# Performance work log

Measured on AMD Instinct MI355X. Metric: run time of the kernel, lower is better.

## Reference

```python
import jax, jax.numpy as jnp
import numpy as np

B, H, T, D, R = 2, 12, 2048, 64, 16
D_STD = D - R


def setup_inputs() -> dict:
    key = jax.random.key(0)
    ks = jax.random.split(key, 5)
    return {
        "Q": jax.random.normal(ks[0], (B, H, T, D), jnp.float32),
        "K": jax.random.normal(ks[1], (B, H, T, D), jnp.float32),
        "V": jax.random.normal(ks[2], (B, H, T, D), jnp.float32),
        "d_bias": jax.random.normal(ks[3], (B, H, T), jnp.float32),
        "W_recip": jax.random.normal(ks[4], (D, R), jnp.float32) * 0.02,
        "w_std": jnp.full((H,), 0.5, jnp.float32),
        "w_rec": jnp.full((H,), 0.3, jnp.float32),
        "w_disc": jnp.full((H,), 0.2, jnp.float32),
    }


def reference(Q, K, V, d_bias, W_recip, w_std, w_rec, w_disc):
    b, h, t, d = Q.shape
    r = W_recip.shape[1]
    d_std = d - r
    sq_std = jnp.sqrt(w_std)[None, :, None, None]  # [1,H,1,1]
    sq_rec = jnp.sqrt(w_rec)[None, :, None, None]
    Q_low = jnp.einsum("bhtd,dr->bhtr", Q, W_recip)  # [B,H,T,R]
    K_low = jnp.einsum("bhtd,dr->bhtr", K, W_recip)
    Q_aug = jnp.concatenate([sq_std * Q[..., :d_std], sq_rec * K_low], axis=-1)  # [B,H,T,D]
    K_aug = jnp.concatenate([sq_std * K[..., :d_std], sq_rec * Q_low], axis=-1)
    scale = 1.0 / jnp.sqrt(jnp.asarray(d, Q.dtype))
    scores = jnp.einsum("bhqd,bhkd->bhqk", Q_aug, K_aug) * scale  # [B,H,T,T]
    # rank-1 additive bias, broadcast over queries: bias[b,h,q,k] = w_disc[h]*d_bias[b,h,k]
    scores = scores + (w_disc[None, :, None, None] * d_bias[:, :, None, :])
    causal = jnp.tril(jnp.ones((t, t), bool))  # [T,T]
    scores = jnp.where(causal[None, None], scores, -jnp.inf)
    attn = jax.nn.softmax(scores, axis=-1)
    return jnp.einsum("bhqk,bhkd->bhqd", attn, V)
```

## Files before the change

kernel.cpp:

```cpp
#include <hip/hip_runtime.h>
#include <math.h>

#define T_SEQ 2048
#define NH    12
#define NB    2
#define BHC   (NB*NH)
#define NQT   32

typedef _Float16 half4_t __attribute__((ext_vector_type(4)));
typedef _Float16 half8_t __attribute__((ext_vector_type(8)));
typedef float    floatx4 __attribute__((ext_vector_type(4)));

__device__ __forceinline__ half8_t h8splat(_Float16 s) {
  return (half8_t){s, s, s, s, s, s, s, s};
}

__global__ __launch_bounds__(256) void prep_kernel(
    const float* __restrict__ Q, const float* __restrict__ K,
    const float* __restrict__ V, const float* __restrict__ W,
    const float* __restrict__ wstd, const float* __restrict__ wrec,
    const float* __restrict__ dbias, const float* __restrict__ wdisc,
    ushort* __restrict__ QF, ushort* __restrict__ KF, ushort* __restrict__ VF,
    float* __restrict__ B2)
{
  __shared__ __align__(16) _Float16 Qsh[64*72];
  __shared__ __align__(16) _Float16 Ksh[64*72];
  __shared__ __align__(16) _Float16 Vsh[64*72];
  __shared__ __align__(16) _Float16 Lqh[64*16];
  __shared__ __align__(16) _Float16 Lkh[64*16];

  const int tid = threadIdx.x;
  const int w = tid >> 6, lane = tid & 63;
  const int quad = lane >> 4, ln = lane & 15;
  const int bh = blockIdx.x >> 5, tblk = blockIdx.x & 31;
  const long g0 = ((long)bh * T_SEQ + tblk * 64) * 64;

  const float4* gQ = (const float4*)(Q + g0);
  const float4* gK = (const float4*)(K + g0);
  const float4* gV = (const float4*)(V + g0);
  for (int i = tid; i < 1024; i += 256) {
    int r = i >> 4, c4 = i & 15;
    float4 q = gQ[i], k = gK[i], v = gV[i];
    *(half4_t*)&Qsh[r*72 + c4*4] = (half4_t){(_Float16)q.x,(_Float16)q.y,(_Float16)q.z,(_Float16)q.w};
    *(half4_t*)&Ksh[r*72 + c4*4] = (half4_t){(_Float16)k.x,(_Float16)k.y,(_Float16)k.z,(_Float16)k.w};
    *(half4_t*)&Vsh[r*72 + c4*4] = (half4_t){(_Float16)v.x,(_Float16)v.y,(_Float16)v.z,(_Float16)v.w};
  }
  __syncthreads();

  half4_t bw[4];
#pragma unroll
  for (int dk = 0; dk < 4; dk++)
#pragma unroll
    for (int i = 0; i < 4; i++)
      bw[dk][i] = (_Float16)W[(dk*16 + quad*4 + i)*16 + ln];

  floatx4 cq = {0.f,0.f,0.f,0.f}, ck = {0.f,0.f,0.f,0.f};
#pragma unroll
  for (int dk = 0; dk < 4; dk++) {
    half4_t aq = *(const half4_t*)&Qsh[(w*16 + ln)*72 + dk*16 + quad*4];
    half4_t ak = *(const half4_t*)&Ksh[(w*16 + ln)*72 + dk*16 + quad*4];
    cq = __builtin_amdgcn_mfma_f32_16x16x16f16(aq, bw[dk], cq, 0, 0, 0);
    ck = __builtin_amdgcn_mfma_f32_16x16x16f16(ak, bw[dk], ck, 0, 0, 0);
  }
#pragma unroll
  for (int i = 0; i < 4; i++) {
    Lqh[(w*16 + quad*4 + i)*16 + ln] = (_Float16)cq[i];
    Lkh[(w*16 + quad*4 + i)*16 + ln] = (_Float16)ck[i];
  }
  __syncthreads();

  const int h = bh % NH;
  const float sstd = sqrtf(wstd[h]);
  const float srec = sqrtf(wrec[h]);
  const half8_t hq_std = h8splat((_Float16)(0.125f * sstd));
  const half8_t hk_std = h8splat((_Float16)sstd);
  const half8_t hq_rec = h8splat((_Float16)(0.125f * srec));
  const half8_t hk_rec = h8splat((_Float16)srec);

  if (tid < 64) B2[(long)bh*T_SEQ + tblk*64 + tid] =
      wdisc[h] * dbias[(long)bh*T_SEQ + tblk*64 + tid];

#pragma unroll
  for (int cc = 0; cc < 2; cc++) {
    int c = tid + cc * 256;
    {
      int lp = c & 63, dp = (c >> 6) & 1, rt = c >> 7;
      int row = rt*16 + (lp & 15);
      int d0 = dp*32 + (lp >> 4)*8;
      half8_t hq, hk;
      if (d0 < 48) {
        hq = *(const half8_t*)&Qsh[row*72 + d0] * hq_std;
        hk = *(const half8_t*)&Ksh[row*72 + d0] * hk_std;
      } else {
        hq = *(const half8_t*)&Lkh[row*16 + (d0-48)] * hq_rec;
        hk = *(const half8_t*)&Lqh[row*16 + (d0-48)] * hk_rec;
      }
      long tile16 = (long)bh*128 + tblk*4 + rt;
      ((int4*)QF)[tile16*128 + dp*64 + lp] = *(int4*)&hq;
      ((int4*)KF)[tile16*128 + dp*64 + lp] = *(int4*)&hk;
    }
    {
      int lv = c & 63, nt = (c >> 6) & 3, v2 = c >> 8;
      int d = nt*16 + (lv & 15), qv = lv >> 4;
      half8_t hv;
#pragma unroll
      for (int j = 0; j < 4; j++) {
        hv[j]   = Vsh[(v2*32 + qv*4 + j)*72 + d];
        hv[4+j] = Vsh[(v2*32 + 16 + qv*4 + j)*72 + d];
      }
      ((int4*)VF)[((long)bh*32 + tblk)*512 + (v2*4 + nt)*64 + lv] = *(int4*)&hv;
    }
  }
}

__global__ __launch_bounds__(64, 4) void flash_kernel(
    const ushort* __restrict__ QF, const ushort* __restrict__ KF,
    const ushort* __restrict__ VF, const float* __restrict__ B2,
    float* __restrict__ Out)
{
  const int lane = threadIdx.x;
  const int quad = lane >> 4, ln = lane & 15;
  const int bid = blockIdx.x;
  const int bh  = bid % BHC;
  const int t16 = 127 - bid / BHC;
  const int qrow = t16*16 + ln;
  const int ktmax = t16 >> 2;

  const ushort* gK = KF + (long)bh * 131072;
  const ushort* gV = VF + (long)bh * 131072;
  const float*  gB = B2 + (long)bh * T_SEQ;

  half8_t bq[2];
  {
    const ushort* gQ = QF + ((long)bh*128 + t16) * 1024;
    bq[0] = *(const half8_t*)(gQ + lane*8);
    bq[1] = *(const half8_t*)(gQ + 512 + lane*8);
  }

  float m_i = -1e30f, l_i = 0.f;
  floatx4 acc[4];
#pragma unroll
  for (int nt = 0; nt < 4; nt++) acc[nt] = (floatx4){0.f,0.f,0.f,0.f};

  for (int kt = 0; kt <= ktmax; kt++) {
    const ushort* Kt = gK + (long)kt * 4096;
    const ushort* Vt = gV + (long)kt * 4096;

    floatx4 st[4];
#pragma unroll
    for (int mt = 0; mt < 4; mt++) {
      half8_t a0 = *(const half8_t*)(Kt + (mt*2    )*512 + lane*8);
      half8_t a1 = *(const half8_t*)(Kt + (mt*2 + 1)*512 + lane*8);
      floatx4 c = (floatx4){0.f,0.f,0.f,0.f};
      c = __builtin_amdgcn_mfma_f32_16x16x32_f16(a0, bq[0], c, 0, 0, 0);
      c = __builtin_amdgcn_mfma_f32_16x16x32_f16(a1, bq[1], c, 0, 0, 0);
      st[mt] = c;
    }

    const bool diag = (kt == ktmax);
    float rowmax = -1e30f;
#pragma unroll
    for (int mt = 0; mt < 4; mt++) {
      float4 bb = *(const float4*)(gB + kt*64 + mt*16 + quad*4);
      float bv[4] = {bb.x, bb.y, bb.z, bb.w};
#pragma unroll
      for (int i = 0; i < 4; i++) {
        float v = st[mt][i] + bv[i];
        int key = kt*64 + mt*16 + quad*4 + i;
        if (diag && key > qrow) v = -1e30f;
        st[mt][i] = v;
        rowmax = fmaxf(rowmax, v);
      }
    }
    rowmax = fmaxf(rowmax, __shfl_xor(rowmax, 16));
    rowmax = fmaxf(rowmax, __shfl_xor(rowmax, 32));
    float mnew  = fmaxf(m_i, rowmax);
    float alpha = __expf(m_i - mnew);
    float psum = 0.f;
    half4_t pa[4];
#pragma unroll
    for (int mt = 0; mt < 4; mt++)
#pragma unroll
      for (int i = 0; i < 4; i++) {
        float p = __expf(st[mt][i] - mnew);
        psum += p;
        pa[mt][i] = (_Float16)p;
      }
    psum += __shfl_xor(psum, 16);
    psum += __shfl_xor(psum, 32);
    l_i = l_i * alpha + psum;
    m_i = mnew;

    float af[4];
#pragma unroll
    for (int i = 0; i < 4; i++) af[i] = __shfl(alpha, quad*4 + i);
#pragma unroll
    for (int nt = 0; nt < 4; nt++)
#pragma unroll
      for (int i = 0; i < 4; i++) acc[nt][i] *= af[i];

#pragma unroll
    for (int v2 = 0; v2 < 2; v2++)
#pragma unroll
      for (int nt = 0; nt < 4; nt++) {
        half8_t vv = *(const half8_t*)(Vt + (v2*4 + nt)*512 + lane*8);
        half4_t b0 = __builtin_shufflevector(vv, vv, 0,1,2,3);
        half4_t b1 = __builtin_shufflevector(vv, vv, 4,5,6,7);
        acc[nt] = __builtin_amdgcn_mfma_f32_16x16x16f16(pa[2*v2],   b0, acc[nt], 0, 0, 0);
        acc[nt] = __builtin_amdgcn_mfma_f32_16x16x16f16(pa[2*v2+1], b1, acc[nt], 0, 0, 0);
      }
  }

  float lr[4];
#pragma unroll
  for (int i = 0; i < 4; i++) lr[i] = 1.f / __shfl(l_i, quad*4 + i);
  const long obase = (long)bh*T_SEQ*64 + (long)(t16*16)*64;
#pragma unroll
  for (int i = 0; i < 4; i++)
#pragma unroll
    for (int nt = 0; nt < 4; nt++)
      Out[obase + (quad*4 + i)*64 + nt*16 + ln] = acc[nt][i] * lr[i];
}

extern "C" void kernel_launch(void* const* d_in, const int* in_sizes, int n_in,
                              void* d_out, int out_size, void* d_ws, size_t ws_size,
                              hipStream_t stream) {
  const float* Q     = (const float*)d_in[0];
  const float* K     = (const float*)d_in[1];
  const float* V     = (const float*)d_in[2];
  const float* dbias = (const float*)d_in[3];
  const float* W     = (const float*)d_in[4];
  const float* wstd  = (const float*)d_in[5];
  const float* wrec  = (const float*)d_in[6];
  const float* wdisc = (const float*)d_in[7];
  float* Out = (float*)d_out;

  const long NEL = (long)BHC * T_SEQ * 64;
  ushort* QF = (ushort*)d_ws;
  ushort* KF = QF + NEL;
  ushort* VF = KF + NEL;
  float*  B2 = (float*)(VF + NEL);

  prep_kernel<<<BHC * NQT, 256, 0, stream>>>(Q, K, V, W, wstd, wrec, dbias, wdisc,
                                             QF, KF, VF, B2);
  flash_kernel<<<BHC * 128, 64, 0, stream>>>(QF, KF, VF, B2, Out);
}
```

Measured before the change: 135.3 us.

## Process two 16-row query tiles per wavefront to reuse K/V loads

Each flash wavefront now handles 32 query rows (two 16-row tiles) instead of 16, sharing every K and V fragment load between two sets of MFMAs and softmax states. This halves global K/V traffic per query and gives more independent MFMA chains to hide latency. In exchange it halves the grid size, roughly doubles register use (the occupancy hint in launch bounds is dropped), and the upper tile in each pair does some extra masked work on the diagonal block.

```diff
diff --git a/kernel.cpp b/kernel.cpp
--- a/kernel.cpp
+++ b/kernel.cpp
@@ -113,7 +113,7 @@
   }
 }
 
-__global__ __launch_bounds__(64, 4) void flash_kernel(
+__global__ __launch_bounds__(64) void flash_kernel(
     const ushort* __restrict__ QF, const ushort* __restrict__ KF,
     const ushort* __restrict__ VF, const float* __restrict__ B2,
     float* __restrict__ Out)
@@ -122,82 +122,101 @@
   const int quad = lane >> 4, ln = lane & 15;
   const int bid = blockIdx.x;
   const int bh  = bid % BHC;
-  const int t16 = 127 - bid / BHC;
-  const int qrow = t16*16 + ln;
-  const int ktmax = t16 >> 2;
+  const int u   = 63 - bid / BHC;
+  const int qrow_a = 32*u + ln;
+  const int qrow_b = qrow_a + 16;
+  const int ktmax = u >> 1;
 
   const ushort* gK = KF + (long)bh * 131072;
   const ushort* gV = VF + (long)bh * 131072;
   const float*  gB = B2 + (long)bh * T_SEQ;
 
-  half8_t bq[2];
+  half8_t bqa[2], bqb[2];
   {
-    const ushort* gQ = QF + ((long)bh*128 + t16) * 1024;
-    bq[0] = *(const half8_t*)(gQ + lane*8);
-    bq[1] = *(const half8_t*)(gQ + 512 + lane*8);
-  }
-
-  float m_i = -1e30f, l_i = 0.f;
-  floatx4 acc[4];
-#pragma unroll
-  for (int nt = 0; nt < 4; nt++) acc[nt] = (floatx4){0.f,0.f,0.f,0.f};
+    const ushort* gQa = QF + ((long)bh*128 + 2*u) * 1024;
+    bqa[0] = *(const half8_t*)(gQa + lane*8);
+    bqa[1] = *(const half8_t*)(gQa + 512 + lane*8);
+    bqb[0] = *(const half8_t*)(gQa + 1024 + lane*8);
+    bqb[1] = *(const half8_t*)(gQa + 1536 + lane*8);
+  }
+
+  float m_a = -1e30f, l_a = 0.f, m_b = -1e30f, l_b = 0.f;
+  floatx4 acca[4], accb[4];
+#pragma unroll
+  for (int nt = 0; nt < 4; nt++) {
+    acca[nt] = (floatx4){0.f,0.f,0.f,0.f};
+    accb[nt] = (floatx4){0.f,0.f,0.f,0.f};
+  }
 
   for (int kt = 0; kt <= ktmax; kt++) {
     const ushort* Kt = gK + (long)kt * 4096;
     const ushort* Vt = gV + (long)kt * 4096;
 
-    floatx4 st[4];
+    floatx4 sta[4], stb[4];
 #pragma unroll
     for (int mt = 0; mt < 4; mt++) {
       half8_t a0 = *(const half8_t*)(Kt + (mt*2    )*512 + lane*8);
       half8_t a1 = *(const half8_t*)(Kt + (mt*2 + 1)*512 + lane*8);
-      floatx4 c = (floatx4){0.f,0.f,0.f,0.f};
-      c = __builtin_amdgcn_mfma_f32_16x16x32_f16(a0, bq[0], c, 0, 0, 0);
-      c = __builtin_amdgcn_mfma_f32_16x16x32_f16(a1, bq[1], c, 0, 0, 0);
-      st[mt] = c;
+      floatx4 ca = (floatx4){0.f,0.f,0.f,0.f};
+      floatx4 cb = (floatx4){0.f,0.f,0.f,0.f};
+      ca = __builtin_amdgcn_mfma_f32_16x16x32_f16(a0, bqa[0], ca, 0, 0, 0);
+      cb = __builtin_amdgcn_mfma_f32_16x16x32_f16(a0, bqb[0], cb, 0, 0, 0);
+      ca = __builtin_amdgcn_mfma_f32_16x16x32_f16(a1, bqa[1], ca, 0, 0, 0);
+      cb = __builtin_amdgcn_mfma_f32_16x16x32_f16(a1, bqb[1], cb, 0, 0, 0);
+      sta[mt] = ca; stb[mt] = cb;
     }
 
     const bool diag = (kt == ktmax);
-    float rowmax = -1e30f;
+    float rma = -1e30f, rmb = -1e30f;
 #pragma unroll
     for (int mt = 0; mt < 4; mt++) {
       float4 bb = *(const float4*)(gB + kt*64 + mt*16 + quad*4);
       float bv[4] = {bb.x, bb.y, bb.z, bb.w};
 #pragma unroll
       for (int i = 0; i < 4; i++) {
-        float v = st[mt][i] + bv[i];
         int key = kt*64 + mt*16 + quad*4 + i;
-        if (diag && key > qrow) v = -1e30f;
-        st[mt][i] = v;
-        rowmax = fmaxf(rowmax, v);
-      }
-    }
-    rowmax = fmaxf(rowmax, __shfl_xor(rowmax, 16));
-    rowmax = fmaxf(rowmax, __shfl_xor(rowmax, 32));
-    float mnew  = fmaxf(m_i, rowmax);
-    float alpha = __expf(m_i - mnew);
-    float psum = 0.f;
-    half4_t pa[4];
+        float va = sta[mt][i] + bv[i];
+        float vb = stb[mt][i] + bv[i];
+        if (diag && key > qrow_a) va = -1e30f;
+        if (diag && key > qrow_b) vb = -1e30f;
+        sta[mt][i] = va; stb[mt][i] = vb;
+        rma = fmaxf(rma, va); rmb = fmaxf(rmb, vb);
+      }
+    }
+    rma = fmaxf(rma, __shfl_xor(rma, 16)); rma = fmaxf(rma, __shfl_xor(rma, 32));
+    rmb = fmaxf(rmb, __shfl_xor(rmb, 16)); rmb = fmaxf(rmb, __shfl_xor(rmb, 32));
+    float mna = fmaxf(m_a, rma), mnb = fmaxf(m_b, rmb);
+    float ala = __expf(m_a - mna), alb = __expf(m_b - mnb);
+    float psa = 0.f, psb = 0.f;
+    half4_t paa[4], pab[4];
 #pragma unroll
     for (int mt = 0; mt < 4; mt++)
 #pragma unroll
       for (int i = 0; i < 4; i++) {
-        float p = __expf(st[mt][i] - mnew);
-        psum += p;
-        pa[mt][i] = (_Float16)p;
-      }
-    psum += __shfl_xor(psum, 16);
-    psum += __shfl_xor(psum, 32);
-    l_i = l_i * alpha + psum;
-    m_i = mnew;
-
-    float af[4];
-#pragma unroll
-    for (int i = 0; i < 4; i++) af[i] = __shfl(alpha, quad*4 + i);
+        float pa = __expf(sta[mt][i] - mna);
+        float pb = __expf(stb[mt][i] - mnb);
+        psa += pa; psb += pb;
+        paa[mt][i] = (_Float16)pa;
+        pab[mt][i] = (_Float16)pb;
+      }
+    psa += __shfl_xor(psa, 16); psa += __shfl_xor(psa, 32);
+    psb += __shfl_xor(psb, 16); psb += __shfl_xor(psb, 32);
+    l_a = l_a * ala + psa;  m_a = mna;
+    l_b = l_b * alb + psb;  m_b = mnb;
+
+    float afa[4], afb[4];
+#pragma unroll
+    for (int i = 0; i < 4; i++) {
+      afa[i] = __shfl(ala, quad*4 + i);
+      afb[i] = __shfl(alb, quad*4 + i);
+    }
 #pragma unroll
     for (int nt = 0; nt < 4; nt++)
 #pragma unroll
-      for (int i = 0; i < 4; i++) acc[nt][i] *= af[i];
+      for (int i = 0; i < 4; i++) {
+        acca[nt][i] *= afa[i];
+        accb[nt][i] *= afb[i];
+      }
 
 #pragma unroll
     for (int v2 = 0; v2 < 2; v2++)
@@ -206,20 +225,27 @@
         half8_t vv = *(const half8_t*)(Vt + (v2*4 + nt)*512 + lane*8);
         half4_t b0 = __builtin_shufflevector(vv, vv, 0,1,2,3);
         half4_t b1 = __builtin_shufflevector(vv, vv, 4,5,6,7);
-        acc[nt] = __builtin_amdgcn_mfma_f32_16x16x16f16(pa[2*v2],   b0, acc[nt], 0, 0, 0);
-        acc[nt] = __builtin_amdgcn_mfma_f32_16x16x16f16(pa[2*v2+1], b1, acc[nt], 0, 0, 0);
-      }
-  }
-
-  float lr[4];
-#pragma unroll
-  for (int i = 0; i < 4; i++) lr[i] = 1.f / __shfl(l_i, quad*4 + i);
-  const long obase = (long)bh*T_SEQ*64 + (long)(t16*16)*64;
+        acca[nt] = __builtin_amdgcn_mfma_f32_16x16x16f16(paa[2*v2],   b0, acca[nt], 0, 0, 0);
+        accb[nt] = __builtin_amdgcn_mfma_f32_16x16x16f16(pab[2*v2],   b0, accb[nt], 0, 0, 0);
+        acca[nt] = __builtin_amdgcn_mfma_f32_16x16x16f16(paa[2*v2+1], b1, acca[nt], 0, 0, 0);
+        accb[nt] = __builtin_amdgcn_mfma_f32_16x16x16f16(pab[2*v2+1], b1, accb[nt], 0, 0, 0);
+      }
+  }
+
+  float lra[4], lrb[4];
+#pragma unroll
+  for (int i = 0; i < 4; i++) {
+    lra[i] = 1.f / __shfl(l_a, quad*4 + i);
+    lrb[i] = 1.f / __shfl(l_b, quad*4 + i);
+  }
+  const long obase = (long)bh*T_SEQ*64 + (long)(32*u)*64;
 #pragma unroll
   for (int i = 0; i < 4; i++)
 #pragma unroll
-    for (int nt = 0; nt < 4; nt++)
-      Out[obase + (quad*4 + i)*64 + nt*16 + ln] = acc[nt][i] * lr[i];
+    for (int nt = 0; nt < 4; nt++) {
+      Out[obase + (quad*4 + i)*64        + nt*16 + ln] = acca[nt][i] * lra[i];
+      Out[obase + (16 + quad*4 + i)*64   + nt*16 + ln] = accb[nt][i] * lrb[i];
+    }
 }
 
 extern "C" void kernel_launch(void* const* d_in, const int* in_sizes, int n_in,
@@ -243,5 +269,5 @@
 
   prep_kernel<<<BHC * NQT, 256, 0, stream>>>(Q, K, V, W, wstd, wrec, dbias, wdisc,
                                              QF, KF, VF, B2);
-  flash_kernel<<<BHC * 128, 64, 0, stream>>>(QF, KF, VF, B2, Out);
-}
+  flash_kernel<<<BHC * 64, 64, 0, stream>>>(QF, KF, VF, B2, Out);
+}
```

After: 223.6 us. 1.65x slower.

## Split causal attention along the KV axis into chunks and merge partial results

Applied to the files above, without the earlier changes.

Flash attention is restructured as split-KV. Causal work is divided into chunks of 8 key tiles, with diagonal and off-diagonal blocks scheduled separately over 256-thread blocks. Partial outputs are stored in fp16 together with m/l statistics, and a new merge kernel combines them. Smaller changes come along: log2e is folded into the Q scale and bias so exp2f can be used, the bias is preloaded into the MFMA accumulator, and K/V fragments are loaded ahead of use. The aim is better load balance and occupancy, at the cost of an extra kernel launch, workspace traffic, and fp16 rounding of the partials.

```diff
diff --git a/kernel.cpp b/kernel.cpp
--- a/kernel.cpp
+++ b/kernel.cpp
@@ -6,6 +6,7 @@
 #define NB    2
 #define BHC   (NB*NH)
 #define NQT   32
+#define LOG2E 1.44269504088896340736f
 
 typedef _Float16 half4_t __attribute__((ext_vector_type(4)));
 typedef _Float16 half8_t __attribute__((ext_vector_type(8)));
@@ -72,13 +73,14 @@
   const int h = bh % NH;
   const float sstd = sqrtf(wstd[h]);
   const float srec = sqrtf(wrec[h]);
-  const half8_t hq_std = h8splat((_Float16)(0.125f * sstd));
+  const float qsc  = 0.125f * LOG2E;
+  const half8_t hq_std = h8splat((_Float16)(qsc * sstd));
   const half8_t hk_std = h8splat((_Float16)sstd);
-  const half8_t hq_rec = h8splat((_Float16)(0.125f * srec));
+  const half8_t hq_rec = h8splat((_Float16)(qsc * srec));
   const half8_t hk_rec = h8splat((_Float16)srec);
 
   if (tid < 64) B2[(long)bh*T_SEQ + tblk*64 + tid] =
-      wdisc[h] * dbias[(long)bh*T_SEQ + tblk*64 + tid];
+      LOG2E * wdisc[h] * dbias[(long)bh*T_SEQ + tblk*64 + tid];
 
 #pragma unroll
   for (int cc = 0; cc < 2; cc++) {
@@ -113,113 +115,209 @@
   }
 }
 
-__global__ __launch_bounds__(64, 4) void flash_kernel(
+__global__ __launch_bounds__(256, 6) void flash_kernel(
     const ushort* __restrict__ QF, const ushort* __restrict__ KF,
     const ushort* __restrict__ VF, const float* __restrict__ B2,
+    ushort* __restrict__ P, float* __restrict__ ML,
+    float* __restrict__ Out)
+{
+  const int tid = threadIdx.x;
+  const int w = tid >> 6, lane = tid & 63;
+  const int quad = lane >> 4, ln = lane & 15;
+  const int bid = blockIdx.x;
+  const int bh  = bid % BHC;
+  const int rest = bid / BHC;
+  int c, j; bool diag;
+  if (rest < 48) {
+    if (rest < 24)      { c = 0; j = 8 + rest; }
+    else if (rest < 40) { c = 1; j = rest - 16; }
+    else                { c = 2; j = rest - 32; }
+    diag = false;
+  } else {
+    int d = rest - 48;
+    c = d & 3; j = 7 - (d >> 2);
+    diag = true;
+  }
+  const int t16 = 32*c + 4*j + w;
+  const int g   = 8*c + j;
+  const int k0  = 8*c;
+  const int nUn = diag ? j : 8;
+  const int qrow = t16*16 + ln;
+
+  const ushort* gK = KF + (long)bh * 131072;
+  const ushort* gV = VF + (long)bh * 131072;
+  const float*  gB = B2 + (long)bh * T_SEQ;
+
+  half8_t bq[2];
+  {
+    const ushort* gQ = QF + ((long)bh*128 + t16) * 1024;
+    bq[0] = *(const half8_t*)(gQ + lane*8);
+    bq[1] = *(const half8_t*)(gQ + 512 + lane*8);
+  }
+
+  float m_i = -1e30f, l_i = 0.f;
+  floatx4 acc[4];
+#pragma unroll
+  for (int nt = 0; nt < 4; nt++) acc[nt] = (floatx4){0.f,0.f,0.f,0.f};
+
+  auto body = [&](int kt, bool domask) {
+    const ushort* Kt = gK + (long)kt * 4096;
+    const ushort* Vt = gV + (long)kt * 4096;
+    float4 bbc[4];
+#pragma unroll
+    for (int mt = 0; mt < 4; mt++)
+      bbc[mt] = *(const float4*)(gB + kt*64 + mt*16 + quad*4);
+    half8_t kf[8];
+#pragma unroll
+    for (int cc = 0; cc < 8; cc++)
+      kf[cc] = *(const half8_t*)(Kt + cc*512 + lane*8);
+
+    floatx4 st[4];
+#pragma unroll
+    for (int mt = 0; mt < 4; mt++) {
+      floatx4 cc = (floatx4){bbc[mt].x, bbc[mt].y, bbc[mt].z, bbc[mt].w};
+      cc = __builtin_amdgcn_mfma_f32_16x16x32_f16(kf[mt*2],     bq[0], cc, 0, 0, 0);
+      cc = __builtin_amdgcn_mfma_f32_16x16x32_f16(kf[mt*2 + 1], bq[1], cc, 0, 0, 0);
+      st[mt] = cc;
+    }
+    half8_t vf[8];
+#pragma unroll
+    for (int cc = 0; cc < 8; cc++)
+      vf[cc] = *(const half8_t*)(Vt + cc*512 + lane*8);
+
+    float rowmax = -1e30f;
+#pragma unroll
+    for (int mt = 0; mt < 4; mt++)
+#pragma unroll
+      for (int i = 0; i < 4; i++) {
+        float v = st[mt][i];
+        if (domask) { int key = kt*64 + mt*16 + quad*4 + i; if (key > qrow) v = -1e30f; }
+        st[mt][i] = v;
+        rowmax = fmaxf(rowmax, v);
+      }
+    rowmax = fmaxf(rowmax, __shfl_xor(rowmax, 16));
+    rowmax = fmaxf(rowmax, __shfl_xor(rowmax, 32));
+    float mnew  = fmaxf(m_i, rowmax);
+    float alpha = exp2f(m_i - mnew);
+    float psum = 0.f;
+    half4_t pa[4];
+#pragma unroll
+    for (int mt = 0; mt < 4; mt++)
+#pragma unroll
+      for (int i = 0; i < 4; i++) {
+        float p = exp2f(st[mt][i] - mnew);
+        psum += p;
+        pa[mt][i] = (_Float16)p;
+      }
+    psum += __shfl_xor(psum, 16);
+    psum += __shfl_xor(psum, 32);
+    l_i = l_i * alpha + psum;
+    m_i = mnew;
+
+    float af[4];
+#pragma unroll
+    for (int i = 0; i < 4; i++) af[i] = __shfl(alpha, quad*4 + i);
+#pragma unroll
+    for (int nt = 0; nt < 4; nt++)
+#pragma unroll
+      for (int i = 0; i < 4; i++) acc[nt][i] *= af[i];
+
+#pragma unroll
+    for (int v2 = 0; v2 < 2; v2++)
+#pragma unroll
+      for (int nt = 0; nt < 4; nt++) {
+        half8_t vv = vf[v2*4 + nt];
+        half4_t b0 = __builtin_shufflevector(vv, vv, 0,1,2,3);
+        half4_t b1 = __builtin_shufflevector(vv, vv, 4,5,6,7);
+        acc[nt] = __builtin_amdgcn_mfma_f32_16x16x16f16(pa[2*v2],   b0, acc[nt], 0, 0, 0);
+        acc[nt] = __builtin_amdgcn_mfma_f32_16x16x16f16(pa[2*v2+1], b1, acc[nt], 0, 0, 0);
+      }
+  };
+
+  for (int it = 0; it < nUn; it++) body(k0 + it, false);
+  if (diag) body(g, true);
+
+  float lr[4];
+#pragma unroll
+  for (int i = 0; i < 4; i++) lr[i] = 1.f / __shfl(l_i, quad*4 + i);
+
+  if (diag && c == 0) {
+    const long obase = (long)bh*T_SEQ*64 + (long)(t16*16)*64;
+#pragma unroll
+    for (int i = 0; i < 4; i++)
+#pragma unroll
+      for (int nt = 0; nt < 4; nt++)
+        Out[obase + (quad*4 + i)*64 + nt*16 + ln] = acc[nt][i] * lr[i];
+  } else {
+    const int a = t16 >> 5, b = t16 & 31;
+    const int slot = bh*320 + t16 + 16*a*(a-1) + a*b + c;
+    half8_t h0, h1;
+#pragma unroll
+    for (int i = 0; i < 4; i++) {
+      h0[i]   = (_Float16)(acc[0][i] * lr[i]);
+      h0[4+i] = (_Float16)(acc[1][i] * lr[i]);
+      h1[i]   = (_Float16)(acc[2][i] * lr[i]);
+      h1[4+i] = (_Float16)(acc[3][i] * lr[i]);
+    }
+    *(int4*)&P[(long)slot*1024 + lane*16]     = *(int4*)&h0;
+    *(int4*)&P[(long)slot*1024 + lane*16 + 8] = *(int4*)&h1;
+    if (quad == 0) {
+      ML[slot*32 + ln]      = m_i;
+      ML[slot*32 + 16 + ln] = l_i;
+    }
+  }
+}
+
+__global__ __launch_bounds__(64) void merge_kernel(
+    const ushort* __restrict__ P, const float* __restrict__ ML,
     float* __restrict__ Out)
 {
   const int lane = threadIdx.x;
   const int quad = lane >> 4, ln = lane & 15;
   const int bid = blockIdx.x;
-  const int bh  = bid % BHC;
-  const int t16 = 127 - bid / BHC;
-  const int qrow = t16*16 + ln;
-  const int ktmax = t16 >> 2;
-
-  const ushort* gK = KF + (long)bh * 131072;
-  const ushort* gV = VF + (long)bh * 131072;
-  const float*  gB = B2 + (long)bh * T_SEQ;
-
-  half8_t bq[2];
-  {
-    const ushort* gQ = QF + ((long)bh*128 + t16) * 1024;
-    bq[0] = *(const half8_t*)(gQ + lane*8);
-    bq[1] = *(const half8_t*)(gQ + 512 + lane*8);
-  }
-
-  float m_i = -1e30f, l_i = 0.f;
-  floatx4 acc[4];
-#pragma unroll
-  for (int nt = 0; nt < 4; nt++) acc[nt] = (floatx4){0.f,0.f,0.f,0.f};
-
-  for (int kt = 0; kt <= ktmax; kt++) {
-    const ushort* Kt = gK + (long)kt * 4096;
-    const ushort* Vt = gV + (long)kt * 4096;
-
-    floatx4 st[4];
-#pragma unroll
-    for (int mt = 0; mt < 4; mt++) {
-      half8_t a0 = *(const half8_t*)(Kt + (mt*2    )*512 + lane*8);
-      half8_t a1 = *(const half8_t*)(Kt + (mt*2 + 1)*512 + lane*8);
-      floatx4 c = (floatx4){0.f,0.f,0.f,0.f};
-      c = __builtin_amdgcn_mfma_f32_16x16x32_f16(a0, bq[0], c, 0, 0, 0);
-      c = __builtin_amdgcn_mfma_f32_16x16x32_f16(a1, bq[1], c, 0, 0, 0);
-      st[mt] = c;
-    }
-
-    const bool diag = (kt == ktmax);
-    float rowmax = -1e30f;
-#pragma unroll
-    for (int mt = 0; mt < 4; mt++) {
-      float4 bb = *(const float4*)(gB + kt*64 + mt*16 + quad*4);
-      float bv[4] = {bb.x, bb.y, bb.z, bb.w};
-#pragma unroll
-      for (int i = 0; i < 4; i++) {
-        float v = st[mt][i] + bv[i];
-        int key = kt*64 + mt*16 + quad*4 + i;
-        if (diag && key > qrow) v = -1e30f;
-        st[mt][i] = v;
-        rowmax = fmaxf(rowmax, v);
-      }
-    }
-    rowmax = fmaxf(rowmax, __shfl_xor(rowmax, 16));
-    rowmax = fmaxf(rowmax, __shfl_xor(rowmax, 32));
-    float mnew  = fmaxf(m_i, rowmax);
-    float alpha = __expf(m_i - mnew);
-    float psum = 0.f;
-    half4_t pa[4];
-#pragma unroll
-    for (int mt = 0; mt < 4; mt++)
-#pragma unroll
-      for (int i = 0; i < 4; i++) {
-        float p = __expf(st[mt][i] - mnew);
-        psum += p;
-        pa[mt][i] = (_Float16)p;
-      }
-    psum += __shfl_xor(psum, 16);
-    psum += __shfl_xor(psum, 32);
-    l_i = l_i * alpha + psum;
-    m_i = mnew;
-
-    float af[4];
-#pragma unroll
-    for (int i = 0; i < 4; i++) af[i] = __shfl(alpha, quad*4 + i);
+  const int bh = bid % BHC;
+  const int t16 = 32 + bid / BHC;
+  const int a = t16 >> 5, b = t16 & 31;
+  const int S = a + 1;
+  const int slot0 = bh*320 + t16 + 16*a*(a-1) + a*b;
+
+  float mc[4][4], lc[4][4], mstar[4] = {-1e30f,-1e30f,-1e30f,-1e30f};
+  for (int cc = 0; cc < S; cc++)
+#pragma unroll
+    for (int i = 0; i < 4; i++) {
+      mc[cc][i] = ML[(slot0+cc)*32 + quad*4 + i];
+      lc[cc][i] = ML[(slot0+cc)*32 + 16 + quad*4 + i];
+      mstar[i] = fmaxf(mstar[i], mc[cc][i]);
+    }
+  float lsum[4] = {0.f,0.f,0.f,0.f};
+  float wgt[4][4];
+  for (int cc = 0; cc < S; cc++)
+#pragma unroll
+    for (int i = 0; i < 4; i++) {
+      wgt[cc][i] = exp2f(mc[cc][i] - mstar[i]) * lc[cc][i];
+      lsum[i] += wgt[cc][i];
+    }
+
+  float out[16];
+#pragma unroll
+  for (int i = 0; i < 16; i++) out[i] = 0.f;
+  for (int cc = 0; cc < S; cc++) {
+    half8_t h0 = *(const half8_t*)&P[(long)(slot0+cc)*1024 + lane*16];
+    half8_t h1 = *(const half8_t*)&P[(long)(slot0+cc)*1024 + lane*16 + 8];
+#pragma unroll
+    for (int i = 0; i < 4; i++) {
+      out[0*4+i] += wgt[cc][i] * (float)h0[i];
+      out[1*4+i] += wgt[cc][i] * (float)h0[4+i];
+      out[2*4+i] += wgt[cc][i] * (float)h1[i];
+      out[3*4+i] += wgt[cc][i] * (float)h1[4+i];
+    }
+  }
+  const long obase = (long)bh*T_SEQ*64 + (long)(t16*16)*64;
+#pragma unroll
+  for (int i = 0; i < 4; i++)
 #pragma unroll
     for (int nt = 0; nt < 4; nt++)
-#pragma unroll
-      for (int i = 0; i < 4; i++) acc[nt][i] *= af[i];
-
-#pragma unroll
-    for (int v2 = 0; v2 < 2; v2++)
-#pragma unroll
-      for (int nt = 0; nt < 4; nt++) {
-        half8_t vv = *(const half8_t*)(Vt + (v2*4 + nt)*512 + lane*8);
-        half4_t b0 = __builtin_shufflevector(vv, vv, 0,1,2,3);
-        half4_t b1 = __builtin_shufflevector(vv, vv, 4,5,6,7);
-        acc[nt] = __builtin_amdgcn_mfma_f32_16x16x16f16(pa[2*v2],   b0, acc[nt], 0, 0, 0);
-        acc[nt] = __builtin_amdgcn_mfma_f32_16x16x16f16(pa[2*v2+1], b1, acc[nt], 0, 0, 0);
-      }
-  }
-
-  float lr[4];
-#pragma unroll
-  for (int i = 0; i < 4; i++) lr[i] = 1.f / __shfl(l_i, quad*4 + i);
-  const long obase = (long)bh*T_SEQ*64 + (long)(t16*16)*64;
-#pragma unroll
-  for (int i = 0; i < 4; i++)
-#pragma unroll
-    for (int nt = 0; nt < 4; nt++)
-      Out[obase + (quad*4 + i)*64 + nt*16 + ln] = acc[nt][i] * lr[i];
+      Out[obase + (quad*4 + i)*64 + nt*16 + ln] = out[nt*4+i] / lsum[i];
 }
 
 extern "C" void kernel_launch(void* const* d_in, const int* in_sizes, int n_in,
@@ -240,8 +338,11 @@
   ushort* KF = QF + NEL;
   ushort* VF = KF + NEL;
   float*  B2 = (float*)(VF + NEL);
+  ushort* P  = (ushort*)(B2 + (long)BHC*T_SEQ);
+  float*  ML = (float*)(P + (long)7680*1024);
 
   prep_kernel<<<BHC * NQT, 256, 0, stream>>>(Q, K, V, W, wstd, wrec, dbias, wdisc,
                                              QF, KF, VF, B2);
-  flash_kernel<<<BHC * 128, 64, 0, stream>>>(QF, KF, VF, B2, Out);
-}
+  flash_kernel<<<BHC * 80, 256, 0, stream>>>(QF, KF, VF, B2, P, ML, Out);
+  merge_kernel<<<BHC * 96, 64, 0, stream>>>(P, ML, Out);
+}
```

Result: slower. 141.8 us (+4.8%).
